# Performance work log

Measured on AMD Instinct MI355X. Metric: run time of the kernel, lower is better.

Reference implementation:

```python
import jax, jax.numpy as jnp
import numpy as np

# Kernel mus per KNRM._get_kernels_layers with kernel_num=21 (step = 1/20)
_first = np.round([0.05 + i * 0.10 for i in range(10)], 2)
MUS = np.concatenate([-_first[::-1], _first, [1.0]]).astype(np.float32)
SIGMAS = np.where(MUS == 1.0, 0.001, 0.1).astype(np.float32)

B, LQ, LD, VOCAB, D = 1024, 64, 512, 100000, 64


def setup_inputs() -> dict:
    key = jax.random.key(0)
    ks = jax.random.split(key, 11)
    return {
        "query_1": jax.random.randint(ks[0], (B, LQ), 0, VOCAB),
        "doc_1": jax.random.randint(ks[1], (B, LD), 0, VOCAB),
        "query_2": jax.random.randint(ks[2], (B, LQ), 0, VOCAB),
        "doc_2": jax.random.randint(ks[3], (B, LD), 0, VOCAB),
        "emb": jax.random.normal(ks[4], (VOCAB, D), dtype=jnp.float32),
        "w1": jax.random.normal(ks[5], (10, 21), dtype=jnp.float32) * 0.3,
        "b1": jax.random.normal(ks[6], (10,), dtype=jnp.float32) * 0.1,
        "w2": jax.random.normal(ks[7], (5, 10), dtype=jnp.float32) * 0.3,
        "b2": jax.random.normal(ks[8], (5,), dtype=jnp.float32) * 0.1,
        "w3": jax.random.normal(ks[9], (1, 5), dtype=jnp.float32) * 0.3,
        "b3": jax.random.normal(ks[10], (1,), dtype=jnp.float32) * 0.1,
    }


def _l2norm(x):
    # torch F.normalize(p=2, dim=-1): x / max(||x||, 1e-12)
    n = jnp.sqrt(jnp.sum(x * x, axis=-1, keepdims=True))
    return x / jnp.maximum(n, 1e-12)


def _predict(query, doc, emb, w1, b1, w2, b2, w3, b3):
    eq = _l2norm(emb[query])          # [B, Lq, D]
    ed = _l2norm(emb[doc])            # [B, Ld, D]
    mm = jnp.einsum("bld,brd->blr", eq, ed)  # [B, Lq, Ld]
    feats = []
    for mu, sg in zip(MUS, SIGMAS):   # fixed small loop over 21 kernels
        k = jnp.exp(-0.5 * ((mm - mu) / sg) ** 2)     # [B, Lq, Ld]
        feats.append(jnp.sum(jnp.log1p(jnp.sum(k, axis=-1)), axis=-1))  # [B]
    f = jnp.stack(feats, axis=1)      # [B, 21]
    h = jax.nn.relu(f @ w1.T + b1)
    h = jax.nn.relu(h @ w2.T + b2)
    return h @ w3.T + b3              # [B, 1]


def reference(query_1, doc_1, query_2, doc_2, emb, w1, b1, w2, b2, w3, b3):
    l1 = _predict(query_1, doc_1, emb, w1, b1, w2, b2, w3, b3)
    l2 = _predict(query_2, doc_2, emb, w1, b1, w2, b2, w3, b3)
    return jax.nn.sigmoid(l1 - l2)
```

## Files before the change

kernel.cpp:

```cpp
#include <hip/hip_runtime.h>
#include <math.h>

#define NK 21

typedef __attribute__((ext_vector_type(8))) _Float16 half8;
typedef __attribute__((ext_vector_type(4))) float floatx4;
typedef __attribute__((ext_vector_type(2))) float f32x2;

__device__ __forceinline__ float ex2(float x) { return __builtin_amdgcn_exp2f(x); }
__device__ __forceinline__ float rsq(float x) { return __builtin_amdgcn_rsqf(x); }
__device__ __forceinline__ float lg2(float x) { return __builtin_amdgcn_logf(x); }
__device__ __forceinline__ f32x2 bc2(float s) { f32x2 r = {s, s}; return r; }

__global__ __launch_bounds__(256) void knrm_norm_table(
    const float* __restrict__ emb, _Float16* __restrict__ tab, int vocab) {
  const int t = threadIdx.x;
  const int row = blockIdx.x * 32 + (t >> 3);
  const int part = t & 7;
  if (row >= vocab) return;
  const float4* src = (const float4*)(emb + (size_t)row * 64 + part * 8);
  const float4 v0 = src[0], v1 = src[1];
  float ss = v0.x*v0.x + v0.y*v0.y + v0.z*v0.z + v0.w*v0.w
           + v1.x*v1.x + v1.y*v1.y + v1.z*v1.z + v1.w*v1.w;
  ss += __shfl_xor(ss, 1);
  ss += __shfl_xor(ss, 2);
  ss += __shfl_xor(ss, 4);
  const float sc = rsq(fmaxf(ss, 1e-24f));
  half8 hv;
  hv[0] = (_Float16)(v0.x * sc); hv[1] = (_Float16)(v0.y * sc);
  hv[2] = (_Float16)(v0.z * sc); hv[3] = (_Float16)(v0.w * sc);
  hv[4] = (_Float16)(v1.x * sc); hv[5] = (_Float16)(v1.y * sc);
  hv[6] = (_Float16)(v1.z * sc); hv[7] = (_Float16)(v1.w * sc);
  *(half8*)(tab + (size_t)row * 64 + part * 8) = hv;
}

template <bool PRENORM>
__global__ __launch_bounds__(256, 4) void knrm_main(
    const int* __restrict__ q1i, const int* __restrict__ d1i,
    const int* __restrict__ q2i, const int* __restrict__ d2i,
    const float* __restrict__ emb, const _Float16* __restrict__ tab,
    const float* __restrict__ w1, const float* __restrict__ b1,
    const float* __restrict__ w2, const float* __restrict__ b2,
    const float* __restrict__ w3, const float* __restrict__ b3,
    float* __restrict__ logits, int B)
{
  __shared__ _Float16 s_eq[64 * 64];
  __shared__ _Float16 s_ed[64 * 64];
  __shared__ float s_part[4][NK];
  __shared__ float s_F[NK];

  const int t = threadIdx.x;
  const int b = blockIdx.x;
  const int pair = blockIdx.y;
  const int* __restrict__ qid = pair ? q2i : q1i;
  const int* __restrict__ did = pair ? d2i : d1i;

  const float cf = -72.13475204444817f;
  const float c1 = 7.213475204444817f;
  const float A[10] = {
    0.88249690f, 0.32465247f, 0.043936934f, 0.0021874911f, 4.0065260e-5f,
    2.6995838e-7f, 6.6915900e-10f, 6.1022440e-13f, 2.0470720e-16f, 2.5261690e-20f};

#pragma unroll
  for (int n = 0; n < 2; ++n) {
    const int lin = n * 256 + t;
    const int q = lin >> 3;
    const int s = (lin & 7) ^ (q & 7);
    const int id = qid[b * 64 + q];
    if (PRENORM) {
      *(half8*)&s_eq[lin * 8] = *(const half8*)(tab + (size_t)id * 64 + s * 8);
    } else {
      const float4* src = (const float4*)(emb + (size_t)id * 64 + s * 8);
      const float4 v0 = src[0], v1 = src[1];
      float ss = v0.x*v0.x + v0.y*v0.y + v0.z*v0.z + v0.w*v0.w
               + v1.x*v1.x + v1.y*v1.y + v1.z*v1.z + v1.w*v1.w;
      ss += __shfl_xor(ss, 1);
      ss += __shfl_xor(ss, 2);
      ss += __shfl_xor(ss, 4);
      const float sc = rsq(fmaxf(ss, 1e-24f));
      half8 hv;
      hv[0] = (_Float16)(v0.x * sc); hv[1] = (_Float16)(v0.y * sc);
      hv[2] = (_Float16)(v0.z * sc); hv[3] = (_Float16)(v0.w * sc);
      hv[4] = (_Float16)(v1.x * sc); hv[5] = (_Float16)(v1.y * sc);
      hv[6] = (_Float16)(v1.z * sc); hv[7] = (_Float16)(v1.w * sc);
      *(half8*)&s_eq[lin * 8] = hv;
    }
  }

  const int lane = t & 63;
  const int w  = t >> 6;
  const int lr = lane & 15;
  const int lg = lane >> 4;
  const int qrow = w * 16 + lr;

  f32x2 kacc2[20];
#pragma unroll
  for (int i = 0; i < 20; ++i) kacc2[i] = bc2(0.0f);
  float kacc20 = 0.0f;

  half8 af0, af1;

#pragma unroll 1
  for (int ch = 0; ch < 8; ++ch) {
    if (ch) __syncthreads();
#pragma unroll
    for (int n = 0; n < 2; ++n) {
      const int lin = n * 256 + t;
      const int d = lin >> 3;
      const int s = (lin & 7) ^ (d & 7);
      const int id = did[b * 512 + ch * 64 + d];
      if (PRENORM) {
        *(half8*)&s_ed[lin * 8] = *(const half8*)(tab + (size_t)id * 64 + s * 8);
      } else {
        const float4* src = (const float4*)(emb + (size_t)id * 64 + s * 8);
        const float4 v0 = src[0], v1 = src[1];
        float ss = v0.x*v0.x + v0.y*v0.y + v0.z*v0.z + v0.w*v0.w
                 + v1.x*v1.x + v1.y*v1.y + v1.z*v1.z + v1.w*v1.w;
        ss += __shfl_xor(ss, 1);
        ss += __shfl_xor(ss, 2);
        ss += __shfl_xor(ss, 4);
        const float sc = rsq(fmaxf(ss, 1e-24f));
        half8 hv;
        hv[0] = (_Float16)(v0.x * sc); hv[1] = (_Float16)(v0.y * sc);
        hv[2] = (_Float16)(v0.z * sc); hv[3] = (_Float16)(v0.w * sc);
        hv[4] = (_Float16)(v1.x * sc); hv[5] = (_Float16)(v1.y * sc);
        hv[6] = (_Float16)(v1.z * sc); hv[7] = (_Float16)(v1.w * sc);
        *(half8*)&s_ed[lin * 8] = hv;
      }
    }
    __syncthreads();

    if (ch == 0) {
      const int q7 = qrow & 7;
      af0 = *(const half8*)&s_eq[(qrow * 8 + ((0 + lg) ^ q7)) * 8];
      af1 = *(const half8*)&s_eq[(qrow * 8 + ((4 + lg) ^ q7)) * 8];
    }

#pragma unroll
    for (int dt = 0; dt < 4; ++dt) {
      const int drow = dt * 16 + lr;
      const int d7 = drow & 7;
      const half8 b0 = *(const half8*)&s_ed[(drow * 8 + ((0 + lg) ^ d7)) * 8];
      const half8 b1 = *(const half8*)&s_ed[(drow * 8 + ((4 + lg) ^ d7)) * 8];
      floatx4 c = {0.0f, 0.0f, 0.0f, 0.0f};
      c = __builtin_amdgcn_mfma_f32_16x16x32_f16(b0, af0, c, 0, 0, 0);
      c = __builtin_amdgcn_mfma_f32_16x16x32_f16(b1, af1, c, 0, 0, 0);
#pragma unroll
      for (int pr = 0; pr < 2; ++pr) {
        const f32x2 x = {c[2 * pr], c[2 * pr + 1]};
        kacc20 += (x[0] > 0.99f ? 1.0f : 0.0f) + (x[1] > 0.99f ? 1.0f : 0.0f);
        const f32x2 xx = x * x;
        f32x2 u, gp, gn;
        u[0]  = ex2(cf * xx[0]); u[1]  = ex2(cf * xx[1]);
        const f32x2 ag = bc2(c1) * x;
        gp[0] = ex2(ag[0]);  gp[1] = ex2(ag[1]);
        gn[0] = ex2(-ag[0]); gn[1] = ex2(-ag[1]);
        const f32x2 h = gp * gp, rh = gn * gn;
        f32x2 v = u * gp, vn = u * gn;
#pragma unroll
        for (int k = 0; k < 10; ++k) {
          kacc2[10 + k] += v * bc2(A[k]);
          kacc2[9 - k]  += vn * bc2(A[k]);
          if (k < 9) { v *= h; vn *= rh; }
        }
      }
    }
  }

  float F[NK];
#pragma unroll
  for (int i = 0; i < NK; ++i) {
    float v = (i < 20) ? (kacc2[i][0] + kacc2[i][1]) : kacc20;
    v += __shfl_xor(v, 16);
    v += __shfl_xor(v, 32);
    v = 0.6931471805599453f * lg2(1.0f + v);
    v += __shfl_xor(v, 1);
    v += __shfl_xor(v, 2);
    v += __shfl_xor(v, 4);
    v += __shfl_xor(v, 8);
    F[i] = v;
  }
  if (lane == 0) {
#pragma unroll
    for (int i = 0; i < NK; ++i) s_part[w][i] = F[i];
  }
  __syncthreads();

  if (t < NK)
    s_F[t] = s_part[0][t] + s_part[1][t] + s_part[2][t] + s_part[3][t];
  __syncthreads();

  if (t == 0) {
    float h1[10], h2[5];
#pragma unroll
    for (int j = 0; j < 10; ++j) {
      float s = b1[j];
      for (int i = 0; i < NK; ++i) s = fmaf(s_F[i], w1[j * NK + i], s);
      h1[j] = fmaxf(s, 0.0f);
    }
#pragma unroll
    for (int j = 0; j < 5; ++j) {
      float s = b2[j];
#pragma unroll
      for (int i = 0; i < 10; ++i) s = fmaf(h1[i], w2[j * 10 + i], s);
      h2[j] = fmaxf(s, 0.0f);
    }
    float s = b3[0];
#pragma unroll
    for (int j = 0; j < 5; ++j) s = fmaf(h2[j], w3[j], s);
    logits[pair * B + b] = s;
  }
}

__global__ void knrm_finalize(const float* __restrict__ logits,
                              float* __restrict__ out, int B) {
  const int b = blockIdx.x * blockDim.x + threadIdx.x;
  if (b < B) {
    const float d = logits[b] - logits[B + b];
    out[b] = 1.0f / (1.0f + expf(-d));
  }
}

extern "C" void kernel_launch(void* const* d_in, const int* in_sizes, int n_in,
                              void* d_out, int out_size, void* d_ws, size_t ws_size,
                              hipStream_t stream) {
  const int* q1 = (const int*)d_in[0];
  const int* d1 = (const int*)d_in[1];
  const int* q2 = (const int*)d_in[2];
  const int* d2 = (const int*)d_in[3];
  const float* emb = (const float*)d_in[4];
  const float* w1 = (const float*)d_in[5];
  const float* b1 = (const float*)d_in[6];
  const float* w2 = (const float*)d_in[7];
  const float* b2 = (const float*)d_in[8];
  const float* w3 = (const float*)d_in[9];
  const float* b3 = (const float*)d_in[10];

  const int B = in_sizes[0] / 64;
  const int vocab = in_sizes[4] / 64;
  const size_t tab_bytes = (size_t)vocab * 64 * sizeof(_Float16);
  const bool prenorm = ws_size >= tab_bytes + (size_t)2 * B * sizeof(float) + 256;

  dim3 grid(B, 2);
  if (prenorm) {
    _Float16* tab = (_Float16*)d_ws;
    float* logits = (float*)((char*)d_ws + ((tab_bytes + 255) & ~(size_t)255));
    knrm_norm_table<<<(vocab + 31) / 32, 256, 0, stream>>>(emb, tab, vocab);
    knrm_main<true><<<grid, 256, 0, stream>>>(q1, d1, q2, d2, emb, tab,
                                              w1, b1, w2, b2, w3, b3, logits, B);
    knrm_finalize<<<(B + 255) / 256, 256, 0, stream>>>(logits, (float*)d_out, B);
  } else {
    float* logits = (float*)d_ws;
    knrm_main<false><<<grid, 256, 0, stream>>>(q1, d1, q2, d2, emb, nullptr,
                                               w1, b1, w2, b2, w3, b3, logits, B);
    knrm_finalize<<<(B + 255) / 256, 256, 0, stream>>>(logits, (float*)d_out, B);
  }
}
```

Before: 97.78 us.

## Load doc embeddings directly into MFMA registers, skipping shared-memory staging

In the prenormalized path, each wave now reads its doc embedding fragments straight from the global fp16 table into registers for the MFMA. This replaces the cooperative LDS staging and the per-chunk __syncthreads, so the doc LDS buffer shrinks to a stub. The grid is flattened to 1D with pair interleaved (b = bid>>1), so the two pairs for a batch item are scheduled next to each other. In exchange, every wave issues its own uncoalesced 16-byte gathers per row, duplicated across the 4 waves, which depends on L2 hits to avoid extra traffic.

```diff
diff --git a/kernel.cpp b/kernel.cpp
--- a/kernel.cpp
+++ b/kernel.cpp
@@ -45,13 +45,14 @@
     float* __restrict__ logits, int B)
 {
   __shared__ _Float16 s_eq[64 * 64];
-  __shared__ _Float16 s_ed[64 * 64];
+  __shared__ _Float16 s_ed[PRENORM ? 8 : 64 * 64];
   __shared__ float s_part[4][NK];
   __shared__ float s_F[NK];
 
   const int t = threadIdx.x;
-  const int b = blockIdx.x;
-  const int pair = blockIdx.y;
+  const int bid = blockIdx.x;
+  const int b = bid >> 1;
+  const int pair = bid & 1;
   const int* __restrict__ qid = pair ? q2i : q1i;
   const int* __restrict__ did = pair ? d2i : d1i;
 
@@ -86,6 +87,7 @@
       *(half8*)&s_eq[lin * 8] = hv;
     }
   }
+  __syncthreads();
 
   const int lane = t & 63;
   const int w  = t >> 6;
@@ -98,20 +100,55 @@
   for (int i = 0; i < 20; ++i) kacc2[i] = bc2(0.0f);
   float kacc20 = 0.0f;
 
-  half8 af0, af1;
-
+  const int q7 = qrow & 7;
+  const half8 af0 = *(const half8*)&s_eq[(qrow * 8 + ((0 + lg) ^ q7)) * 8];
+  const half8 af1 = *(const half8*)&s_eq[(qrow * 8 + ((4 + lg) ^ q7)) * 8];
+
+  auto chain = [&](const floatx4& c) {
+#pragma unroll
+    for (int pr = 0; pr < 2; ++pr) {
+      const f32x2 x = {c[2 * pr], c[2 * pr + 1]};
+      kacc20 += (x[0] > 0.99f ? 1.0f : 0.0f) + (x[1] > 0.99f ? 1.0f : 0.0f);
+      const f32x2 xx = x * x;
+      f32x2 u, gp, gn;
+      u[0]  = ex2(cf * xx[0]); u[1]  = ex2(cf * xx[1]);
+      const f32x2 ag = bc2(c1) * x;
+      gp[0] = ex2(ag[0]);  gp[1] = ex2(ag[1]);
+      gn[0] = ex2(-ag[0]); gn[1] = ex2(-ag[1]);
+      const f32x2 h = gp * gp, rh = gn * gn;
+      f32x2 v = u * gp, vn = u * gn;
+#pragma unroll
+      for (int k = 0; k < 10; ++k) {
+        kacc2[10 + k] += v * bc2(A[k]);
+        kacc2[9 - k]  += vn * bc2(A[k]);
+        if (k < 9) { v *= h; vn *= rh; }
+      }
+    }
+  };
+
+  if constexpr (PRENORM) {
+    const int* __restrict__ dbase = did + b * 512;
+#pragma unroll 2
+    for (int dt = 0; dt < 32; ++dt) {
+      const int id = dbase[dt * 16 + lr];
+      const _Float16* rp = tab + (size_t)id * 64 + lg * 8;
+      const half8 b0 = *(const half8*)rp;
+      const half8 b1 = *(const half8*)(rp + 32);
+      floatx4 c = {0.0f, 0.0f, 0.0f, 0.0f};
+      c = __builtin_amdgcn_mfma_f32_16x16x32_f16(b0, af0, c, 0, 0, 0);
+      c = __builtin_amdgcn_mfma_f32_16x16x32_f16(b1, af1, c, 0, 0, 0);
+      chain(c);
+    }
+  } else {
 #pragma unroll 1
-  for (int ch = 0; ch < 8; ++ch) {
-    if (ch) __syncthreads();
-#pragma unroll
-    for (int n = 0; n < 2; ++n) {
-      const int lin = n * 256 + t;
-      const int d = lin >> 3;
-      const int s = (lin & 7) ^ (d & 7);
-      const int id = did[b * 512 + ch * 64 + d];
-      if (PRENORM) {
-        *(half8*)&s_ed[lin * 8] = *(const half8*)(tab + (size_t)id * 64 + s * 8);
-      } else {
+    for (int ch = 0; ch < 8; ++ch) {
+      if (ch) __syncthreads();
+#pragma unroll
+      for (int n = 0; n < 2; ++n) {
+        const int lin = n * 256 + t;
+        const int d = lin >> 3;
+        const int s = (lin & 7) ^ (d & 7);
+        const int id = did[b * 512 + ch * 64 + d];
         const float4* src = (const float4*)(emb + (size_t)id * 64 + s * 8);
         const float4 v0 = src[0], v1 = src[1];
         float ss = v0.x*v0.x + v0.y*v0.y + v0.z*v0.z + v0.w*v0.w
@@ -127,42 +164,17 @@
         hv[6] = (_Float16)(v1.z * sc); hv[7] = (_Float16)(v1.w * sc);
         *(half8*)&s_ed[lin * 8] = hv;
       }
-    }
-    __syncthreads();
-
-    if (ch == 0) {
-      const int q7 = qrow & 7;
-      af0 = *(const half8*)&s_eq[(qrow * 8 + ((0 + lg) ^ q7)) * 8];
-      af1 = *(const half8*)&s_eq[(qrow * 8 + ((4 + lg) ^ q7)) * 8];
-    }
-
-#pragma unroll
-    for (int dt = 0; dt < 4; ++dt) {
-      const int drow = dt * 16 + lr;
-      const int d7 = drow & 7;
-      const half8 b0 = *(const half8*)&s_ed[(drow * 8 + ((0 + lg) ^ d7)) * 8];
-      const half8 b1 = *(const half8*)&s_ed[(drow * 8 + ((4 + lg) ^ d7)) * 8];
-      floatx4 c = {0.0f, 0.0f, 0.0f, 0.0f};
-      c = __builtin_amdgcn_mfma_f32_16x16x32_f16(b0, af0, c, 0, 0, 0);
-      c = __builtin_amdgcn_mfma_f32_16x16x32_f16(b1, af1, c, 0, 0, 0);
-#pragma unroll
-      for (int pr = 0; pr < 2; ++pr) {
-        const f32x2 x = {c[2 * pr], c[2 * pr + 1]};
-        kacc20 += (x[0] > 0.99f ? 1.0f : 0.0f) + (x[1] > 0.99f ? 1.0f : 0.0f);
-        const f32x2 xx = x * x;
-        f32x2 u, gp, gn;
-        u[0]  = ex2(cf * xx[0]); u[1]  = ex2(cf * xx[1]);
-        const f32x2 ag = bc2(c1) * x;
-        gp[0] = ex2(ag[0]);  gp[1] = ex2(ag[1]);
-        gn[0] = ex2(-ag[0]); gn[1] = ex2(-ag[1]);
-        const f32x2 h = gp * gp, rh = gn * gn;
-        f32x2 v = u * gp, vn = u * gn;
-#pragma unroll
-        for (int k = 0; k < 10; ++k) {
-          kacc2[10 + k] += v * bc2(A[k]);
-          kacc2[9 - k]  += vn * bc2(A[k]);
-          if (k < 9) { v *= h; vn *= rh; }
-        }
+      __syncthreads();
+#pragma unroll
+      for (int dt = 0; dt < 4; ++dt) {
+        const int drow = dt * 16 + lr;
+        const int d7 = drow & 7;
+        const half8 b0 = *(const half8*)&s_ed[(drow * 8 + ((0 + lg) ^ d7)) * 8];
+        const half8 b1 = *(const half8*)&s_ed[(drow * 8 + ((4 + lg) ^ d7)) * 8];
+        floatx4 c = {0.0f, 0.0f, 0.0f, 0.0f};
+        c = __builtin_amdgcn_mfma_f32_16x16x32_f16(b0, af0, c, 0, 0, 0);
+        c = __builtin_amdgcn_mfma_f32_16x16x32_f16(b1, af1, c, 0, 0, 0);
+        chain(c);
       }
     }
   }
@@ -241,18 +253,17 @@
   const size_t tab_bytes = (size_t)vocab * 64 * sizeof(_Float16);
   const bool prenorm = ws_size >= tab_bytes + (size_t)2 * B * sizeof(float) + 256;
 
-  dim3 grid(B, 2);
   if (prenorm) {
     _Float16* tab = (_Float16*)d_ws;
     float* logits = (float*)((char*)d_ws + ((tab_bytes + 255) & ~(size_t)255));
     knrm_norm_table<<<(vocab + 31) / 32, 256, 0, stream>>>(emb, tab, vocab);
-    knrm_main<true><<<grid, 256, 0, stream>>>(q1, d1, q2, d2, emb, tab,
-                                              w1, b1, w2, b2, w3, b3, logits, B);
+    knrm_main<true><<<2 * B, 256, 0, stream>>>(q1, d1, q2, d2, emb, tab,
+                                               w1, b1, w2, b2, w3, b3, logits, B);
     knrm_finalize<<<(B + 255) / 256, 256, 0, stream>>>(logits, (float*)d_out, B);
   } else {
     float* logits = (float*)d_ws;
-    knrm_main<false><<<grid, 256, 0, stream>>>(q1, d1, q2, d2, emb, nullptr,
-                                               w1, b1, w2, b2, w3, b3, logits, B);
+    knrm_main<false><<<2 * B, 256, 0, stream>>>(q1, d1, q2, d2, emb, nullptr,
+                                                w1, b1, w2, b2, w3, b3, logits, B);
     knrm_finalize<<<(B + 255) / 256, 256, 0, stream>>>(logits, (float*)d_out, B);
   }
 }
```

Measured after the change: 102.5 us. +4.8%, slower.
